# Optimization experiments

Hardware: AMD Instinct MI355X
Metric: run time of the kernel (lower is better)

The kernel has to match this reference:

```python
import jax, jax.numpy as jnp
import numpy as np

K = 8  # hardcoded knn_point(8, ...) in the original module


def setup_inputs() -> dict:
    key = jax.random.key(0)
    k1, k2, k3 = jax.random.split(key, 3)
    B, N, S, C = 8, 8192, 2048, 256
    return {
        "xyz": jax.random.normal(k1, (B, 3, N), dtype=jnp.float32),
        "sparse_xyz": jax.random.normal(k2, (B, 3, S), dtype=jnp.float32),
        "sparse_feat": jax.random.normal(k3, (B, C, S), dtype=jnp.float32),
    }


def reference(xyz, sparse_xyz, sparse_feat):
    # xyz: [B,3,N] dense query points; sparse_xyz: [B,3,S]; sparse_feat: [B,C,S]
    B, _, N = xyz.shape
    x = jnp.transpose(xyz, (0, 2, 1))          # [B,N,3]
    sx = jnp.transpose(sparse_xyz, (0, 2, 1))  # [B,S,3]
    sf = jnp.transpose(sparse_feat, (0, 2, 1)) # [B,S,C]

    sqr = (jnp.sum(x * x, axis=-1)[:, :, None]
           + jnp.sum(sx * sx, axis=-1)[:, None, :]
           - 2.0 * jnp.einsum('bnc,bsc->bns', x, sx))

    # K nearest neighbors (smallest distance) -> indices [B,N,K]
    _, idx = jax.lax.top_k(-sqr, K)

    bidx = jnp.arange(B)[:, None, None]
    g_xyz = sx[bidx, idx]                      # gather neighbor coords [B,N,K,3]
    diff = g_xyz - x[:, :, None, :]
    dist = jnp.maximum(jnp.linalg.norm(diff, axis=3), 1e-10)  # [B,N,K]

    inv = 1.0 / dist
    weight = inv / jnp.sum(inv, axis=2, keepdims=True)        # [B,N,K]

    g_feat = sf[bidx, idx]                     # gather neighbor feats [B,N,K,C]
    dense = jnp.sum(weight[..., None] * g_feat, axis=2)       # [B,N,C]
    return jnp.transpose(dense, (0, 2, 1))     # [B,C,N]
```

## Files before the change

### kernel.cpp

```cpp
#include <hip/hip_runtime.h>
#include <hip/hip_fp16.h>

#define BB 8
#define NN 8192
#define SS 2048
#define CC 256
#define KNN 8
#define TOPM 10
#define NLIST 4
#define QPB 64
#define MSTRIDE 41
#define P2STR 66

#define UMIN(a, b) __builtin_elementwise_min(a, b)
#define UMAX(a, b) __builtin_elementwise_max(a, b)

typedef short bf16x8_t __attribute__((ext_vector_type(8)));
typedef float f32x4_t __attribute__((ext_vector_type(4)));

__device__ __forceinline__ float2 unpack_h2(unsigned u) {
    __half2 h = *reinterpret_cast<__half2*>(&u);
    return __half22float2(h);
}

__device__ __forceinline__ unsigned short f2bf(float f) {
    unsigned u = __float_as_uint(f);
    u += 0x7FFFu + ((u >> 16) & 1u);
    return (unsigned short)(u >> 16);
}
__device__ __forceinline__ float bf2f(unsigned short h) {
    return __uint_as_float((unsigned)h << 16);
}

__device__ __forceinline__ unsigned med3u(unsigned a, unsigned b, unsigned c) {
    unsigned d;
    asm("v_med3_u32 %0, %1, %2, %3" : "=v"(d) : "v"(a), "v"(b), "v"(c));
    return d;
}

__device__ __forceinline__ void ins1(unsigned k1[TOPM], unsigned c) {
#pragma unroll
    for (int j = TOPM - 1; j >= 1; --j)
        k1[j] = med3u(c, k1[j - 1], k1[j]);
    k1[0] = UMIN(k1[0], c);
}

__device__ __forceinline__ void ins_step(unsigned k1[TOPM], f32x4_t d, unsigned sbase) {
    ins1(k1, (__float_as_uint(d[0]) & 0xFFFFF800u) | sbase);
    ins1(k1, (__float_as_uint(d[1]) & 0xFFFFF800u) | (sbase + 1u));
    ins1(k1, (__float_as_uint(d[2]) & 0xFFFFF800u) | (sbase + 2u));
    ins1(k1, (__float_as_uint(d[3]) & 0xFFFFF800u) | (sbase + 3u));
}

__global__ __launch_bounds__(256) void prep_kernel(
    const float* __restrict__ sf,
    const float* __restrict__ sxyz,
    unsigned short* __restrict__ sft,
    unsigned short* __restrict__ gt)
{
    __shared__ unsigned short ts[64 * P2STR];

    const int blk = blockIdx.x;
    const int t   = threadIdx.x;

    if (blk < BB * 32 * 4) {
        const int b  = blk & 7;
        const int r  = blk >> 3;
        const int st = r & 31;
        const int c0 = (r >> 5) * 64;

        const int s  = t & 63;
        const int cq = t >> 6;
        const float* sfb = sf + ((long)b * CC + c0) * SS + st * 64;
#pragma unroll
        for (int it = 0; it < 16; ++it) {
            int c = it * 4 + cq;
            float v = sfb[(long)c * SS + s];
            ts[s * P2STR + c] = __half_as_ushort(__float2half_rn(v));
        }
        __syncthreads();

        const int so = t >> 2;
        const int cl = t & 3;
        const unsigned short* src = &ts[so * P2STR + cl * 16];
        unsigned u[8];
#pragma unroll
        for (int i = 0; i < 8; ++i) u[i] = *(const unsigned*)&src[i * 2];
        unsigned short* dst = sft + ((long)b * SS + st * 64 + so) * CC + c0 + cl * 16;
        *(uint4*)&dst[0] = make_uint4(u[0], u[1], u[2], u[3]);
        *(uint4*)&dst[8] = make_uint4(u[4], u[5], u[6], u[7]);
    } else {
        const int idx = blk - BB * 32 * 4;
        const int b = idx & 7;
        const int s = (idx >> 3) * 256 + t;
        const float* sb = sxyz + (long)b * 3 * SS;
        unsigned short* gb = gt + (long)b * 2 * SS * 8;

        float px = sb[s], py = sb[SS + s], pz = sb[2 * SS + s];
        unsigned short xh = f2bf(px); unsigned short xl = f2bf(px - bf2f(xh));
        unsigned short yh = f2bf(py); unsigned short yl = f2bf(py - bf2f(yh));
        unsigned short zh = f2bf(pz); unsigned short zl = f2bf(pz - bf2f(zh));
        float pn = fmaf(px, px, fmaf(py, py, pz * pz));
        unsigned short nh = f2bf(pn); unsigned short nl = f2bf(pn - bf2f(nh));
        const unsigned ONE = 0x3F80u;
        uint4 t0 = make_uint4((unsigned)xh | ((unsigned)xl << 16),
                              (unsigned)xh | ((unsigned)yh << 16),
                              (unsigned)yl | ((unsigned)yh << 16),
                              (unsigned)zh | ((unsigned)zl << 16));
        uint4 t1 = make_uint4((unsigned)zh | ((unsigned)nh << 16),
                              (unsigned)nl | (ONE << 16),
                              ONE | ((unsigned)xl << 16),
                              (unsigned)yl | ((unsigned)zl << 16));
        *(uint4*)&gb[(long)s * 8] = t0;
        *(uint4*)&gb[((long)SS + s) * 8] = t1;
    }
}

__global__ __launch_bounds__(256, 4) void knn_kernel(
    const float* __restrict__ xyz,
    const float* __restrict__ sxyz,
    const unsigned short* __restrict__ gt,
    const unsigned short* __restrict__ sft,
    float* __restrict__ out)
{
    __shared__ unsigned mbuf[QPB * MSTRIDE];
    __shared__ unsigned pk_lds[QPB * KNN];

    const int b    = blockIdx.x & 7;
    const int q0   = (int)(blockIdx.x >> 3) * QPB;
    const int tid  = threadIdx.x;
    const int wave = tid >> 6;
    const int lane = tid & 63;
    const int g    = lane >> 4;
    const int qi   = lane & 15;

    const float* sb = sxyz + (long)b * 3 * SS;
    const float* xb = xyz + (long)b * 3 * NN;

    const int nq = q0 + wave * 16 + qi;
    const float qx = xb[nq], qy = xb[NN + nq], qz = xb[2 * NN + nq];

    bf16x8_t qf = (bf16x8_t)0;
    {
        unsigned short xh = f2bf(qx); float xhf = bf2f(xh);
        unsigned short yh = f2bf(qy); float yhf = bf2f(yh);
        unsigned short zh = f2bf(qz); float zhf = bf2f(zh);
        unsigned short xh2 = f2bf(-2.f * xhf), xl2 = f2bf(-2.f * (qx - xhf));
        unsigned short yh2 = f2bf(-2.f * yhf), yl2 = f2bf(-2.f * (qy - yhf));
        unsigned short zh2 = f2bf(-2.f * zhf), zl2 = f2bf(-2.f * (qz - zhf));
        float qn = fmaf(qx, qx, fmaf(qy, qy, qz * qz)) + 0.0625f;
        unsigned short nh = f2bf(qn); unsigned short nl = f2bf(qn - bf2f(nh));
        const short ONE = (short)0x3F80;
        if (g == 0) {
            qf[0] = (short)xh2; qf[1] = (short)xh2; qf[2] = (short)xl2;
            qf[3] = (short)yh2; qf[4] = (short)yh2; qf[5] = (short)yl2;
            qf[6] = (short)zh2; qf[7] = (short)zh2;
        } else if (g == 1) {
            qf[0] = (short)zl2; qf[1] = ONE; qf[2] = ONE;
            qf[3] = (short)nh;  qf[4] = (short)nl;
            qf[5] = (short)xl2; qf[6] = (short)yl2; qf[7] = (short)zl2;
        }
    }

    const unsigned short* ap =
        gt + (long)b * 2 * SS * 8 + (long)(g & 1) * SS * 8 + qi * 8;

    unsigned k1[TOPM];
#pragma unroll
    for (int j = 0; j < TOPM; ++j) k1[j] = 0xFFFFFFFFu;

    const f32x4_t zacc = {0.f, 0.f, 0.f, 0.f};
    const unsigned ib4 = (unsigned)(g * 4);

    bf16x8_t a0 = *(const bf16x8_t*)ap; ap += 128;
    bf16x8_t a1 = *(const bf16x8_t*)ap; ap += 128;

    for (int step = 0; step < 126; step += 2) {
        f32x4_t d0 = __builtin_amdgcn_mfma_f32_16x16x32_bf16(a0, qf, zacc, 0, 0, 0);
        a0 = *(const bf16x8_t*)ap; ap += 128;
        ins_step(k1, d0, ib4 + (unsigned)(step * 16));
        f32x4_t d1 = __builtin_amdgcn_mfma_f32_16x16x32_bf16(a1, qf, zacc, 0, 0, 0);
        a1 = *(const bf16x8_t*)ap; ap += 128;
        ins_step(k1, d1, ib4 + (unsigned)((step + 1) * 16));
    }
    {
        f32x4_t d0 = __builtin_amdgcn_mfma_f32_16x16x32_bf16(a0, qf, zacc, 0, 0, 0);
        ins_step(k1, d0, ib4 + (unsigned)(126 * 16));
        f32x4_t d1 = __builtin_amdgcn_mfma_f32_16x16x32_bf16(a1, qf, zacc, 0, 0, 0);
        ins_step(k1, d1, ib4 + (unsigned)(127 * 16));
    }

    {
        unsigned* m1 = &mbuf[(wave * 16 + qi) * MSTRIDE + g * TOPM];
#pragma unroll
        for (int j = 0; j < TOPM; ++j) m1[j] = k1[j];
    }
    __syncthreads();

    if (tid < QPB) {
        const int n2 = q0 + tid;
        const unsigned* ml = &mbuf[tid * MSTRIDE];

        unsigned f1[TOPM];
#pragma unroll
        for (int j = 0; j < TOPM; ++j) f1[j] = 0xFFFFFFFFu;
#pragma unroll 4
        for (int j = 0; j < NLIST * TOPM; ++j) ins1(f1, ml[j]);

        const double dqx = (double)xb[n2], dqy = (double)xb[NN + n2], dqz = (double)xb[2 * NN + n2];
        unsigned long long top[KNN];
#pragma unroll
        for (int j = 0; j < KNN; ++j) top[j] = ~0ull;

#pragma unroll
        for (int j = 0; j < TOPM; ++j) {
            int s = f1[j] & 0x7FF;
            float px = sb[s], py = sb[SS + s], pz = sb[2 * SS + s];
            double ex = (double)px - dqx;
            double ey = (double)py - dqy;
            double ez = (double)pz - dqz;
            double dd = ex * ex + ey * ey + ez * ez;
            unsigned long long c =
                (((unsigned long long)__double_as_longlong(dd)) & ~0x7FFull) | (unsigned long long)s;
#pragma unroll
            for (int jj = KNN - 1; jj >= 1; --jj)
                top[jj] = UMIN(UMAX(top[jj - 1], c), top[jj]);
            top[0] = UMIN(top[0], c);
        }

        const float fqx = xb[n2], fqy = xb[NN + n2], fqz = xb[2 * NN + n2];
        int   id[KNN];
        float inv[KNN];
        float ssum = 0.f;
#pragma unroll
        for (int k = 0; k < KNN; ++k) {
            id[k] = (int)(top[k] & 0x7FFull);
            float px = sb[id[k]], py = sb[SS + id[k]], pz = sb[2 * SS + id[k]];
            float dx = px - fqx, dy = py - fqy, dz = pz - fqz;
            float dv = sqrtf(dx * dx + dy * dy + dz * dz);
            dv = fmaxf(dv, 1e-10f);
            inv[k] = 1.0f / dv;
            ssum += inv[k];
        }
        const float rs = 1.0f / ssum;
#pragma unroll
        for (int k = 0; k < KNN; ++k) {
            unsigned hw = (unsigned)__half_as_ushort(__float2half_rn(inv[k] * rs));
            pk_lds[tid * KNN + k] = (hw << 16) | (unsigned)id[k];
        }
    }
    __syncthreads();

    {
        const int q  = tid >> 2;
        const int cl = tid & 3;
        const unsigned short* sfb = sft + (long)b * SS * CC;
        float* outq = out + (long)b * CC * NN + (q0 + q);

        float wgt[KNN];
        long  off[KNN];
#pragma unroll
        for (int k = 0; k < KNN; ++k) {
            const unsigned p = pk_lds[q * KNN + k];
            off[k] = (long)(p & 0x7FF) * CC;
            wgt[k] = __half2float(__ushort_as_half((unsigned short)(p >> 16)));
        }

#pragma unroll
        for (int cc = 0; cc < 8; ++cc) {
            const int ch = cc * 32 + cl * 8;
            float acc[8];
#pragma unroll
            for (int j = 0; j < 8; ++j) acc[j] = 0.f;

#pragma unroll
            for (int k = 0; k < KNN; ++k) {
                const float w = wgt[k];
                const uint4 F = *(const uint4*)&sfb[off[k] + ch];
                float2 f0 = unpack_h2(F.x), f1 = unpack_h2(F.y);
                float2 f2 = unpack_h2(F.z), f3 = unpack_h2(F.w);
                acc[0] = fmaf(w, f0.x, acc[0]);
                acc[1] = fmaf(w, f0.y, acc[1]);
                acc[2] = fmaf(w, f1.x, acc[2]);
                acc[3] = fmaf(w, f1.y, acc[3]);
                acc[4] = fmaf(w, f2.x, acc[4]);
                acc[5] = fmaf(w, f2.y, acc[5]);
                acc[6] = fmaf(w, f3.x, acc[6]);
                acc[7] = fmaf(w, f3.y, acc[7]);
            }
#pragma unroll
            for (int j = 0; j < 8; ++j)
                __builtin_nontemporal_store(acc[j], &outq[(long)(ch + j) * NN]);
        }
    }
}

extern "C" void kernel_launch(void* const* d_in, const int* in_sizes, int n_in,
                              void* d_out, int out_size, void* d_ws, size_t ws_size,
                              hipStream_t stream) {
    const float* xyz  = (const float*)d_in[0];
    const float* sxyz = (const float*)d_in[1];
    const float* sf   = (const float*)d_in[2];
    float* out = (float*)d_out;

    unsigned short* gtile = (unsigned short*)d_ws;
    unsigned short* sft   = (unsigned short*)((char*)d_ws + 512 * 1024);

    prep_kernel<<<dim3(BB * 32 * 4 + 64), dim3(256), 0, stream>>>(sf, sxyz, sft, gtile);
    knn_kernel<<<dim3(BB * NN / QPB), dim3(256), 0, stream>>>(xyz, sxyz, gtile, sft, out);
}
```

Baseline: 153.7 us.

## Switch KNN distance MFMA to 32x32x16 with split candidate halves per wave

Replaces the 16x16x32 bf16 MFMA distance tile with a 32x32x16 tile, so each wave handles 32 queries against half of the sparse points (waves split by query pair and candidate half). Each lane now keeps a partial top list from 16 distances per MFMA, and the partial lists are merged through shared memory as before. The aim is to stop wasting MFMA K-depth on zero padding, since the old layout only used two of its four lane groups, and to have every lane do useful insertion work. The cost is a 16-wide accumulator per MFMA and a different candidate index mapping.

Measured after the change: 146.4 us. 1.05x faster.

```diff
diff --git a/kernel.cpp b/kernel.cpp
--- a/kernel.cpp
+++ b/kernel.cpp
@@ -15,8 +15,9 @@
 #define UMIN(a, b) __builtin_elementwise_min(a, b)
 #define UMAX(a, b) __builtin_elementwise_max(a, b)
 
-typedef short bf16x8_t __attribute__((ext_vector_type(8)));
-typedef float f32x4_t __attribute__((ext_vector_type(4)));
+typedef short bf16x8_t  __attribute__((ext_vector_type(8)));
+typedef float f32x4_t   __attribute__((ext_vector_type(4)));
+typedef float f32x16_t  __attribute__((ext_vector_type(16)));
 
 __device__ __forceinline__ float2 unpack_h2(unsigned u) {
     __half2 h = *reinterpret_cast<__half2*>(&u);
@@ -45,11 +46,12 @@
     k1[0] = UMIN(k1[0], c);
 }
 
-__device__ __forceinline__ void ins_step(unsigned k1[TOPM], f32x4_t d, unsigned sbase) {
-    ins1(k1, (__float_as_uint(d[0]) & 0xFFFFF800u) | sbase);
-    ins1(k1, (__float_as_uint(d[1]) & 0xFFFFF800u) | (sbase + 1u));
-    ins1(k1, (__float_as_uint(d[2]) & 0xFFFFF800u) | (sbase + 2u));
-    ins1(k1, (__float_as_uint(d[3]) & 0xFFFFF800u) | (sbase + 3u));
+__device__ __forceinline__ void ins_step16(unsigned k1[TOPM], f32x16_t d, unsigned sbase) {
+#pragma unroll
+    for (int r = 0; r < 16; ++r) {
+        unsigned idx = sbase + (unsigned)((r & 3) + 8 * (r >> 2));
+        ins1(k1, (__float_as_uint(d[r]) & 0xFFFFF800u) | idx);
+    }
 }
 
 __global__ __launch_bounds__(256) void prep_kernel(
@@ -131,16 +133,18 @@
     const int tid  = threadIdx.x;
     const int wave = tid >> 6;
     const int lane = tid & 63;
-    const int g    = lane >> 4;
-    const int qi   = lane & 15;
+    const int p    = wave & 1;
+    const int sh   = wave >> 1;
+    const int qc   = lane & 31;
+    const int h    = lane >> 5;
 
     const float* sb = sxyz + (long)b * 3 * SS;
     const float* xb = xyz + (long)b * 3 * NN;
 
-    const int nq = q0 + wave * 16 + qi;
+    const int nq = q0 + p * 32 + qc;
     const float qx = xb[nq], qy = xb[NN + nq], qz = xb[2 * NN + nq];
 
-    bf16x8_t qf = (bf16x8_t)0;
+    bf16x8_t qf;
     {
         unsigned short xh = f2bf(qx); float xhf = bf2f(xh);
         unsigned short yh = f2bf(qy); float yhf = bf2f(yh);
@@ -151,11 +155,11 @@
         float qn = fmaf(qx, qx, fmaf(qy, qy, qz * qz)) + 0.0625f;
         unsigned short nh = f2bf(qn); unsigned short nl = f2bf(qn - bf2f(nh));
         const short ONE = (short)0x3F80;
-        if (g == 0) {
+        if (h == 0) {
             qf[0] = (short)xh2; qf[1] = (short)xh2; qf[2] = (short)xl2;
             qf[3] = (short)yh2; qf[4] = (short)yh2; qf[5] = (short)yl2;
             qf[6] = (short)zh2; qf[7] = (short)zh2;
-        } else if (g == 1) {
+        } else {
             qf[0] = (short)zl2; qf[1] = ONE; qf[2] = ONE;
             qf[3] = (short)nh;  qf[4] = (short)nl;
             qf[5] = (short)xl2; qf[6] = (short)yl2; qf[7] = (short)zl2;
@@ -163,35 +167,37 @@
     }
 
     const unsigned short* ap =
-        gt + (long)b * 2 * SS * 8 + (long)(g & 1) * SS * 8 + qi * 8;
+        gt + (long)b * 2 * SS * 8 + (long)h * SS * 8 + ((long)sh * 1024 + qc) * 8;
 
     unsigned k1[TOPM];
 #pragma unroll
     for (int j = 0; j < TOPM; ++j) k1[j] = 0xFFFFFFFFu;
 
-    const f32x4_t zacc = {0.f, 0.f, 0.f, 0.f};
-    const unsigned ib4 = (unsigned)(g * 4);
-
-    bf16x8_t a0 = *(const bf16x8_t*)ap; ap += 128;
-    bf16x8_t a1 = *(const bf16x8_t*)ap; ap += 128;
-
-    for (int step = 0; step < 126; step += 2) {
-        f32x4_t d0 = __builtin_amdgcn_mfma_f32_16x16x32_bf16(a0, qf, zacc, 0, 0, 0);
-        a0 = *(const bf16x8_t*)ap; ap += 128;
-        ins_step(k1, d0, ib4 + (unsigned)(step * 16));
-        f32x4_t d1 = __builtin_amdgcn_mfma_f32_16x16x32_bf16(a1, qf, zacc, 0, 0, 0);
-        a1 = *(const bf16x8_t*)ap; ap += 128;
-        ins_step(k1, d1, ib4 + (unsigned)((step + 1) * 16));
+    const f32x16_t zacc = (f32x16_t)0.f;
+    const unsigned sb0 = (unsigned)(sh * 1024 + 4 * h);
+
+    bf16x8_t a0 = *(const bf16x8_t*)ap;
+    bf16x8_t a1 = *(const bf16x8_t*)(ap + 256);
+    ap += 512;
+
+    for (int step = 0; step < 30; step += 2) {
+        f32x16_t d0 = __builtin_amdgcn_mfma_f32_32x32x16_bf16(a0, qf, zacc, 0, 0, 0);
+        a0 = *(const bf16x8_t*)ap;
+        ins_step16(k1, d0, sb0 + (unsigned)(step * 32));
+        f32x16_t d1 = __builtin_amdgcn_mfma_f32_32x32x16_bf16(a1, qf, zacc, 0, 0, 0);
+        a1 = *(const bf16x8_t*)(ap + 256);
+        ap += 512;
+        ins_step16(k1, d1, sb0 + (unsigned)((step + 1) * 32));
     }
     {
-        f32x4_t d0 = __builtin_amdgcn_mfma_f32_16x16x32_bf16(a0, qf, zacc, 0, 0, 0);
-        ins_step(k1, d0, ib4 + (unsigned)(126 * 16));
-        f32x4_t d1 = __builtin_amdgcn_mfma_f32_16x16x32_bf16(a1, qf, zacc, 0, 0, 0);
-        ins_step(k1, d1, ib4 + (unsigned)(127 * 16));
+        f32x16_t d0 = __builtin_amdgcn_mfma_f32_32x32x16_bf16(a0, qf, zacc, 0, 0, 0);
+        ins_step16(k1, d0, sb0 + (unsigned)(30 * 32));
+        f32x16_t d1 = __builtin_amdgcn_mfma_f32_32x32x16_bf16(a1, qf, zacc, 0, 0, 0);
+        ins_step16(k1, d1, sb0 + (unsigned)(31 * 32));
     }
 
     {
-        unsigned* m1 = &mbuf[(wave * 16 + qi) * MSTRIDE + g * TOPM];
+        unsigned* m1 = &mbuf[(p * 32 + qc) * MSTRIDE + (sh * 2 + h) * TOPM];
 #pragma unroll
         for (int j = 0; j < TOPM; ++j) m1[j] = k1[j];
     }
@@ -261,9 +267,9 @@
         long  off[KNN];
 #pragma unroll
         for (int k = 0; k < KNN; ++k) {
-            const unsigned p = pk_lds[q * KNN + k];
-            off[k] = (long)(p & 0x7FF) * CC;
-            wgt[k] = __half2float(__ushort_as_half((unsigned short)(p >> 16)));
+            const unsigned pk = pk_lds[q * KNN + k];
+            off[k] = (long)(pk & 0x7FF) * CC;
+            wgt[k] = __half2float(__ushort_as_half((unsigned short)(pk >> 16)));
         }
 
 #pragma unroll
```
